# Performance work log

Hardware: AMD Instinct MI355X
Metric: run time of the kernel (lower is better)

The kernel has to match this reference:

```python
import jax, jax.numpy as jnp
import numpy as np

NHID = 256
NHEADS = 8
HEAD_F = NHID // NHEADS  # GAT per-head out_features
ALPHA = 0.1              # GAT LeakyReLU slope
NEG = -9e15


def _leaky(x, slope):
    return jnp.where(x >= 0, x, slope * x)


def _cnorm(x, axis):
    # matches Norm.compute_norm: (x - mean) / (std_unbiased + 1e-6)
    m = jnp.mean(x, axis=axis, keepdims=True)
    s = jnp.std(x, axis=axis, keepdims=True, ddof=1)
    return (x - m) / (s + 1e-6)


def _norm(x):
    # Norm('bn') forward: per-sample normalize over features (dim=1 of x[i]) then nodes (dim=0)
    return _cnorm(_cnorm(x, axis=2), axis=1)


def setup_inputs() -> dict:
    key = jax.random.key(0)
    ks = jax.random.split(key, 12)
    B, N, E, H, D = 4, 1024, NHID, NHEADS, HEAD_F

    def xavier(k, shape, gain=1.414):
        fan_in, fan_out = shape[-2], shape[-1]
        a = gain * np.sqrt(6.0 / (fan_in + fan_out))
        return jax.random.uniform(k, shape, jnp.float32, -a, a)

    return {
        "x": jax.random.normal(ks[0], (B, N, E), jnp.float32),
        "src": jax.random.normal(ks[1], (N, B, E), jnp.float32),
        "adj": jax.random.randint(ks[2], (B, N, N), 0, 2, jnp.int32),
        "Wg": xavier(ks[3], (H, E, D)),                 # per-head GAT W
        "a1": xavier(ks[4], (H, D, 1))[..., 0],         # a[:D]
        "a2": xavier(ks[5], (H, D, 1))[..., 0],         # a[D:]
        "lin_w": xavier(ks[6], (E, E), gain=1.0),
        "lin_b": jnp.zeros((E,), jnp.float32),
        "in_proj_w": xavier(ks[7], (3 * E, E), gain=1.0),
        "in_proj_b": jnp.zeros((3 * E,), jnp.float32),
        "out_proj_w": xavier(ks[8], (E, E), gain=1.0),
        "out_proj_b": jnp.zeros((E,), jnp.float32),
    }


def reference(x, src, adj, Wg, a1, a2, lin_w, lin_b, in_proj_w, in_proj_b, out_proj_w, out_proj_b):
    B, N, E = x.shape
    H, D = NHEADS, HEAD_F

    # --- multi-head dense GAT (all heads vectorized) ---
    Wh = jnp.einsum("bnf,hfd->hbnd", x, Wg)                      # [H,B,N,D]
    s1 = jnp.einsum("hbnd,hd->hbn", Wh, a1)                      # a1 . Wh_i
    s2 = jnp.einsum("hbnd,hd->hbn", Wh, a2)                      # a2 . Wh_j
    e = _leaky(s1[..., :, None] + s2[..., None, :], ALPHA)       # [H,B,N,N]
    e = jnp.where(adj[None] > 0, e, NEG)
    attn = jax.nn.softmax(e, axis=-1)                            # [H,B,N,N]
    hp = _leaky(jnp.einsum("hbnm,hbmd->hbnd", attn, Wh), 0.01)   # F.leaky_relu default

    x = x + jnp.transpose(hp, (1, 2, 0, 3)).reshape(B, N, H * D)
    e_out = jnp.mean(attn, axis=0)                               # [B,N,N]

    # --- norm1 -> linear -> norm2 ---
    x = _norm(x) @ lin_w.T + lin_b
    x = _norm(x)

    # --- nn.MultiheadAttention(query=x, key=x, value=src) ---
    srcb = jnp.transpose(src, (1, 0, 2))                         # [B,N,E]
    Wq, Wk, Wv = in_proj_w[:E], in_proj_w[E:2 * E], in_proj_w[2 * E:]
    bq, bk, bv = in_proj_b[:E], in_proj_b[E:2 * E], in_proj_b[2 * E:]
    Dh = E // H
    q = (x @ Wq.T + bq).reshape(B, N, H, Dh)
    k = (x @ Wk.T + bk).reshape(B, N, H, Dh)
    v = (srcb @ Wv.T + bv).reshape(B, N, H, Dh)
    scores = jnp.einsum("bqhd,bkhd->bhqk", q, k) / jnp.sqrt(jnp.float32(Dh))
    p = jax.nn.softmax(scores, axis=-1)
    o = jnp.einsum("bhqk,bkhd->bqhd", p, v).reshape(B, N, E)
    x = o @ out_proj_w.T + out_proj_b                            # [B,N,E]

    return (x, e_out)
```

## Files before the change

### kernel.cpp

```cpp
#include <hip/hip_runtime.h>
#include <hip/hip_bf16.h>

#define BIAS_OFF 196608
#define S1_OFF   198400
#define S2_OFF   231168
#define CS_OFF   263936
#define ST1_OFF  296704
#define ST2_OFF  298752
#define A_OFF    300800
#define MX_OFF   825088
#define RS_OFF   857856
#define PK_OFF   890624
#define B_OFF    1349376
#define C_OFF    2397952
#define FLAG_F   3446528

#define NEGC (-9.0e15f)

typedef __attribute__((ext_vector_type(8))) short bf16x8s;
typedef __attribute__((ext_vector_type(4))) float f32x4;

static __device__ __forceinline__ float bf2f(unsigned short u) {
  union { unsigned int i; float f; } v; v.i = ((unsigned int)u) << 16; return v.f;
}
static __device__ __forceinline__ unsigned short f2bf(float f) {
  union { float f; unsigned int u; } v; v.f = f;
  unsigned int r = (v.u + 0x7FFFu + ((v.u >> 16) & 1u)) >> 16;
  return (unsigned short)r;
}
static __device__ __forceinline__ float ldin(const void* p, long i, int bf) {
  return bf ? bf2f(((const unsigned short*)p)[i]) : ((const float*)p)[i];
}
static __device__ __forceinline__ unsigned short rdbf(const void* p, long i, int bf) {
  if (bf) return ((const unsigned short*)p)[i];
  return f2bf(((const float*)p)[i]);
}
static __device__ __forceinline__ void stout(void* p, long i, float v, int bf) {
  if (bf) ((unsigned short*)p)[i] = f2bf(v);
  else    ((float*)p)[i] = v;
}

__global__ __launch_bounds__(64) void detect_kernel(const unsigned short* x, int* flag) {
  int lane = threadIdx.x;
  unsigned short u = x[2 * lane];
  int e = (u >> 7) & 0xFF;
  bool good = (e >= 100 && e <= 140);
  unsigned long long m = __ballot(good);
  if (lane == 0) *flag = (__popcll(m) >= 48) ? 1 : 0;
}

__global__ __launch_bounds__(256) void packadj_kernel(const int* adj,
                                                      unsigned long long* pk) {
  int t = threadIdx.x, w = t >> 6, lane = t & 63;
  long row = blockIdx.x;
  #pragma unroll
  for (int j = 0; j < 4; ++j) {
    int m = t + 256*j;
    bool bit = adj[row*1024 + m] > 0;
    unsigned long long mask = __ballot(bit);
    if (lane == 0) pk[row*16 + w + 4*j] = mask;
  }
}

__global__ __launch_bounds__(256) void prep_kernel(
    const void* wg, const void* lin_w, const void* inp_w, const void* out_w,
    const void* lin_b, const void* inp_b, const void* out_b,
    const void* a1, const void* a2, float* ws, const int* flagp) {
  const int bf = *flagp;
  unsigned short* wbf = (unsigned short*)ws;
  int t = threadIdx.x;
  int f = blockIdx.x;
  int m = blockIdx.y;
  if (m == 0) {
    int h = t >> 5, d = t & 31;
    wbf[t*256 + f] = rdbf(wg, h*8192 + f*32 + d, bf);
  } else if (m <= 5) {
    int dst = m*65536 + t*256 + f;
    if (m == 1)      wbf[dst] = rdbf(lin_w, t*256 + f, bf);
    else if (m == 2) wbf[dst] = rdbf(inp_w, t*256 + f, bf);
    else if (m == 3) wbf[dst] = rdbf(inp_w, (256 + t)*256 + f, bf);
    else if (m == 4) wbf[dst] = rdbf(inp_w, (512 + t)*256 + f, bf);
    else             wbf[dst] = rdbf(out_w, t*256 + f, bf);
  } else {
    int h = t >> 5, d = t & 31;
    float wv = ldin(wg, h*8192 + f*32 + d, bf);
    float p1 = wv * ldin(a1, t, bf);
    float p2 = wv * ldin(a2, t, bf);
    #pragma unroll
    for (int off = 16; off > 0; off >>= 1) {
      p1 += __shfl_xor(p1, off, 32);
      p2 += __shfl_xor(p2, off, 32);
    }
    if (d == 0) {
      ws[CS_OFF + h*256 + f]        = p1;
      ws[CS_OFF + 2048 + h*256 + f] = p2;
    }
    if (f == 0) {
      ws[BIAS_OFF + t]        = ldin(lin_b, t, bf);
      ws[BIAS_OFF + 256 + t]  = ldin(inp_b, t, bf);
      ws[BIAS_OFF + 512 + t]  = ldin(inp_b, 256 + t, bf);
      ws[BIAS_OFF + 768 + t]  = ldin(inp_b, 512 + t, bf);
      ws[BIAS_OFF + 1024 + t] = ldin(out_b, t, bf);
      ws[CS_OFF + 4096 + t]   = 0.0f;
    }
  }
}

__global__ __launch_bounds__(256) void s1s2_kernel(const void* x, float* ws,
                                                   const int* flagp) {
  const int bf = *flagp;
  int t = threadIdx.x;
  int r0 = blockIdx.x * 16;
  __shared__ float X[16][260];
  __shared__ float CA[16][260];
  #pragma unroll
  for (int r = 0; r < 16; ++r)
    X[r][t] = ldin(x, (long)(r0 + r)*256 + t, bf);
  #pragma unroll
  for (int i = 0; i < 16; ++i)
    CA[i][t] = ws[CS_OFF + ((i < 8) ? i*256 : 2048 + (i - 8)*256) + t];
  __syncthreads();
  int r = t >> 4, c = t & 15;
  float acc = 0.0f;
  for (int e = 0; e < 256; ++e) acc += X[r][e] * CA[c][e];
  int row = r0 + r;
  if (c < 8) ws[S1_OFF + c*4096 + row] = acc;
  else       ws[S2_OFF + (c - 8)*4096 + row] = acc;
}

#define PB_S 1032
__global__ __launch_bounds__(512) void attn1a_kernel(const void* x, float* ws,
                                                     const int* flagp) {
  const int bf = *flagp;
  int t = threadIdx.x;
  int gid = blockIdx.x;
  int h = gid & 7;
  int b = (gid >> 3) & 3;
  int n0 = (gid >> 5) * 32;
  __shared__ __align__(16) unsigned char arena[4096 + 32*PB_S*2];
  float* s2s = (float*)arena;
  unsigned short (*Pb)[PB_S] = (unsigned short (*)[PB_S])(arena + 4096);
  float (*opart)[32][17] = (float (*)[32][17])arena;
  int w = t >> 6, lane = t & 63;
  int m = lane & 15, quad = lane >> 4;
  const unsigned long long* pk = (const unsigned long long*)(ws + PK_OFF);
  const float* s2p = ws + S2_OFF + h*4096 + b*1024;
  #pragma unroll
  for (int j = 0; j < 2; ++j) s2s[t + 512*j] = s2p[t + 512*j];
  __syncthreads();
  #pragma unroll
  for (int rr = 0; rr < 4; ++rr) {
    int r = 4*w + rr;
    int rowi = __builtin_amdgcn_readfirstlane(b*1024 + n0 + r);
    const unsigned long long* prow = pk + (long)rowi * 16;
    float s1v = ws[S1_OFF + h*4096 + rowi];
    float p[16];
    float mx = -3.4e38f;
    #pragma unroll
    for (int j = 0; j < 16; ++j) {
      int mm = lane + 64*j;
      float ev = s1v + s2s[mm];
      ev = (ev >= 0.0f) ? ev : 0.1f*ev;
      ev = ((prow[j] >> lane) & 1ull) ? ev : NEGC;
      p[j] = ev;
      mx = fmaxf(mx, ev);
    }
    #pragma unroll
    for (int off = 32; off > 0; off >>= 1) mx = fmaxf(mx, __shfl_xor(mx, off));
    float s = 0.0f;
    #pragma unroll
    for (int j = 0; j < 16; ++j) { p[j] = __expf(p[j] - mx); s += p[j]; }
    #pragma unroll
    for (int off = 32; off > 0; off >>= 1) s += __shfl_xor(s, off);
    float rs = 1.0f / s;
    #pragma unroll
    for (int j = 0; j < 16; ++j)
      Pb[r][lane + 64*j] = f2bf(p[j] * rs);
    if (lane == 0) {
      ws[MX_OFF + h*4096 + rowi] = mx;
      ws[RS_OFF + h*4096 + rowi] = rs;
    }
  }
  __syncthreads();
  f32x4 g0, g1;
  {
    const unsigned short* wht = (const unsigned short*)(ws + A_OFF);
    int ntile = w & 1;
    int ktbase = (w >> 1) * 8;
    int vd = ntile*16 + m;
    const unsigned short* wrow = wht + ((long)((b*8 + h)*32 + vd))*1024;
    f32x4 a0g0 = {0,0,0,0}, a1g0 = {0,0,0,0};
    f32x4 a0g1 = {0,0,0,0}, a1g1 = {0,0,0,0};
    #pragma unroll
    for (int kt2 = 0; kt2 < 4; ++kt2) {
      int kt = ktbase + 2*kt2;
      bf16x8s bw0 = *(const bf16x8s*)(wrow + kt*32 + quad*8);
      bf16x8s bw1 = *(const bf16x8s*)(wrow + (kt+1)*32 + quad*8);
      bf16x8s p00 = *(const bf16x8s*)&Pb[m][kt*32 + quad*8];
      bf16x8s p01 = *(const bf16x8s*)&Pb[16 + m][kt*32 + quad*8];
      a0g0 = __builtin_amdgcn_mfma_f32_16x16x32_bf16(p00, bw0, a0g0, 0, 0, 0);
      a0g1 = __builtin_amdgcn_mfma_f32_16x16x32_bf16(p01, bw0, a0g1, 0, 0, 0);
      bf16x8s p10 = *(const bf16x8s*)&Pb[m][(kt+1)*32 + quad*8];
      bf16x8s p11 = *(const bf16x8s*)&Pb[16 + m][(kt+1)*32 + quad*8];
      a1g0 = __builtin_amdgcn_mfma_f32_16x16x32_bf16(p10, bw1, a1g0, 0, 0, 0);
      a1g1 = __builtin_amdgcn_mfma_f32_16x16x32_bf16(p11, bw1, a1g1, 0, 0, 0);
    }
    g0 = a0g0 + a1g0;
    g1 = a0g1 + a1g1;
  }
  __syncthreads();
  #pragma unroll
  for (int i = 0; i < 4; ++i) {
    opart[w][quad*4 + i][m]      = g0[i];
    opart[w][16 + quad*4 + i][m] = g1[i];
  }
  __syncthreads();
  #pragma unroll
  for (int half = 0; half < 2; ++half) {
    int r = (t >> 5) + half*16;
    int dd = t & 31;
    int nt = dd >> 4, c = dd & 15;
    float sum = opart[nt][r][c] + opart[nt + 2][r][c]
              + opart[nt + 4][r][c] + opart[nt + 6][r][c];
    float hv = (sum >= 0.0f) ? sum : 0.01f*sum;
    long idx = (long)(b*1024 + n0 + r)*256 + h*32 + dd;
    ws[C_OFF + idx] = ldin(x, idx, bf) + hv;
  }
}

__global__ __launch_bounds__(256) void eout_kernel(float* ws, void* dout,
                                                   const int* flagp) {
  const int bf = *flagp;
  int t = threadIdx.x;
  int gid = blockIdx.x;
  int b = gid & 3;
  int n = gid >> 2;
  int row = b*1024 + n;
  int w = t >> 6, lane = t & 63;
  __shared__ float part[8];
  const unsigned long long* pk = (const unsigned long long*)(ws + PK_OFF);
  const unsigned long long* prow = pk + (long)row * 16;
  float v = ws[C_OFF + (long)row*256 + t];
  float s = v;
  #pragma unroll
  for (int off = 32; off > 0; off >>= 1) s += __shfl_xor(s, off);
  if (lane == 0) part[w] = s;
  __syncthreads();
  float mean = (part[0] + part[1] + part[2] + part[3]) * (1.0f/256.0f);
  float d = v - mean;
  float ss = d*d;
  #pragma unroll
  for (int off = 32; off > 0; off >>= 1) ss += __shfl_xor(ss, off);
  if (lane == 0) part[4 + w] = ss;
  __syncthreads();
  float inv = 1.0f / (sqrtf((part[4]+part[5]+part[6]+part[7]) * (1.0f/255.0f)) + 1e-6f);
  ws[B_OFF + (long)row*256 + t] = d * inv;
  float s1v[8], mxv[8], rsv[8];
  #pragma unroll
  for (int h = 0; h < 8; ++h) {
    s1v[h] = ws[S1_OFF + h*4096 + row];
    mxv[h] = ws[MX_OFF + h*4096 + row];
    rsv[h] = ws[RS_OFF + h*4096 + row];
  }
  const float* s2b = ws + S2_OFF + b*1024;
  #pragma unroll
  for (int j = 0; j < 4; ++j) {
    int m = t + 256*j;
    bool a = (prow[w + 4*j] >> lane) & 1ull;
    float acc = 0.0f;
    #pragma unroll
    for (int h = 0; h < 8; ++h) {
      float ev = s1v[h] + s2b[h*4096 + m];
      ev = (ev >= 0.0f) ? ev : 0.1f*ev;
      ev = a ? ev : NEGC;
      acc += rsv[h] * __expf(ev - mxv[h]);
    }
    stout(dout, 1048576L + (long)row*1024 + m, 0.125f*acc, bf);
  }
}

__global__ __launch_bounds__(256) void colstatsA_kernel(const float* in, float* cs) {
  int t = threadIdx.x;
  int j = blockIdx.x & 63;
  int b = blockIdx.x >> 6;
  float s = 0, ss = 0;
  for (int n = j*16; n < j*16 + 16; ++n) {
    float v = in[(b*1024 + n)*256 + t];
    s += v; ss += v*v;
  }
  cs[(b*64 + j)*256 + t] = s;
  cs[65536 + (b*64 + j)*256 + t] = ss;
}

__global__ __launch_bounds__(256) void colstatsB_kernel(const float* cs, float* st) {
  int t = threadIdx.x;
  int b = blockIdx.x;
  float s = 0, ss = 0;
  for (int j = 0; j < 64; ++j) {
    s  += cs[(b*64 + j)*256 + t];
    ss += cs[65536 + (b*64 + j)*256 + t];
  }
  float mean = s * (1.0f/1024.0f);
  float var = fmaxf((ss - s*mean) * (1.0f/1023.0f), 0.0f);
  st[b*256 + t] = mean;
  st[1024 + b*256 + t] = 1.0f / (sqrtf(var) + 1e-6f);
}

template<int IN_MODE, int RN, int OUTM, int CS>
__global__ __launch_bounds__(512) void gemm2_kernel(const void* inp,
    const unsigned short* wmat, const unsigned short* wmat2,
    const float* bias, const float* bias2, const float* st,
    void* outp, float* csout, const int* flagp) {
  const int bf = *flagp;
  int t = threadIdx.x;
  int gid = blockIdx.x;
  int rowg = (CS == 2) ? (gid >> 1) : gid;
  int colbase = (CS == 2) ? ((gid & 1) * 128) : 0;
  int r0 = rowg * 16;
  __shared__ __align__(16) unsigned short Usm[2*16*264];
  unsigned short (*Uh)[264] = (unsigned short (*)[264])Usm;
  unsigned short (*Ul)[264] = (unsigned short (*)[264])(Usm + 16*264);
  {
    int srow = t >> 5;
    int e0 = (t & 31) * 8;
    long grow = r0 + srow;
    float v[8];
    if (IN_MODE == 0) {
      #pragma unroll
      for (int j = 0; j < 8; ++j) v[j] = ldin(inp, grow*256 + e0 + j, bf);
    } else if (IN_MODE == 1) {
      int b = (int)(grow >> 10);
      const float* ip = (const float*)inp + grow*256 + e0;
      const float* mp = st + b*256 + e0;
      const float* vp = st + 1024 + b*256 + e0;
      #pragma unroll
      for (int j = 0; j < 8; ++j) v[j] = (ip[j] - mp[j]) * vp[j];
    } else if (IN_MODE == 2) {
      int b = (int)(grow >> 10), n = (int)(grow & 1023);
      #pragma unroll
      for (int j = 0; j < 8; ++j)
        v[j] = ldin(inp, (long)(n*4 + b)*256 + e0 + j, bf);
    } else {
      int b = (int)(grow >> 10), n = (int)(grow & 1023);
      const float* ip = (const float*)inp
          + ((long)(b*8 + (e0 >> 5))*1024 + n)*32 + (e0 & 31);
      #pragma unroll
      for (int j = 0; j < 8; ++j) v[j] = ip[j];
    }
    unsigned short hv[8], lv[8];
    #pragma unroll
    for (int j = 0; j < 8; ++j) {
      hv[j] = f2bf(v[j]);
      lv[j] = f2bf(v[j] - bf2f(hv[j]));
    }
    *(bf16x8s*)&Uh[srow][e0] = *(bf16x8s*)hv;
    *(bf16x8s*)&Ul[srow][e0] = *(bf16x8s*)lv;
  }
  __syncthreads();
  int w = t >> 6, lane = t & 63, m = lane & 15, quad = lane >> 4;
  const int NT = (CS == 1) ? 2 : 1;
  f32x4 accs[2];
  f32x4 acck;
  #pragma unroll
  for (int nt = 0; nt < NT; ++nt) {
    int o = colbase + w*16 + nt*128 + m;
    const unsigned short* wp = wmat + o*256 + quad*8;
    f32x4 ah_acc = {0,0,0,0}, al_acc = {0,0,0,0};
    f32x4 kh_acc = {0,0,0,0}, kl_acc = {0,0,0,0};
    const unsigned short* wp2 = (OUTM == 5) ? (wmat2 + o*256 + quad*8) : wp;
    #pragma unroll
    for (int kt = 0; kt < 8; ++kt) {
      bf16x8s ah = *(const bf16x8s*)&Uh[m][kt*32 + quad*8];
      bf16x8s al = *(const bf16x8s*)&Ul[m][kt*32 + quad*8];
      bf16x8s bw = *(const bf16x8s*)(wp + kt*32);
      ah_acc = __builtin_amdgcn_mfma_f32_16x16x32_bf16(ah, bw, ah_acc, 0, 0, 0);
      al_acc = __builtin_amdgcn_mfma_f32_16x16x32_bf16(al, bw, al_acc, 0, 0, 0);
      if (OUTM == 5) {
        bf16x8s bw2 = *(const bf16x8s*)(wp2 + kt*32);
        kh_acc = __builtin_amdgcn_mfma_f32_16x16x32_bf16(ah, bw2, kh_acc, 0, 0, 0);
        kl_acc = __builtin_amdgcn_mfma_f32_16x16x32_bf16(al, bw2, kl_acc, 0, 0, 0);
      }
    }
    accs[nt] = ah_acc + al_acc;
    if (OUTM == 5) acck = kh_acc + kl_acc;
    if (RN == 0) {
      float bv = bias[o];
      if constexpr (OUTM == 0) {
        #pragma unroll
        for (int i = 0; i < 4; ++i) {
          long row = r0 + quad*4 + i;
          ((float*)outp)[row*256 + o] = accs[nt][i] + bv;
        }
      } else if constexpr (OUTM == 1) {
        #pragma unroll
        for (int i = 0; i < 4; ++i) {
          long row = r0 + quad*4 + i;
          stout(outp, row*256 + o, accs[nt][i] + bv, bf);
        }
      } else if constexpr (OUTM == 4) {
        int h = o >> 5, d = o & 31;
        #pragma unroll
        for (int i = 0; i < 4; ++i) {
          long row = r0 + quad*4 + i;
          int b = (int)(row >> 10), n = (int)(row & 1023);
          ((unsigned short*)outp)[((long)((b*8 + h)*32 + d))*1024 + n]
              = f2bf(accs[nt][i] + bv);
        }
      } else if constexpr (OUTM == 5) {
        float* wsf = (float*)outp;
        float* qhm = wsf + A_OFF;
        unsigned short* khm = (unsigned short*)(wsf + B_OFF);
        float bq = bias[o], bk = bias2[o];
        int h = o >> 5, d = o & 31;
        #pragma unroll
        for (int i = 0; i < 4; ++i) {
          long row = r0 + quad*4 + i;
          int b = (int)(row >> 10), n = (int)(row & 1023);
          long idx = ((long)((b*8 + h)*1024 + n))*32 + d;
          qhm[idx] = accs[nt][i] + bq;
          khm[idx] = f2bf(acck[i] + bk);
        }
      }
    }
  }
  if constexpr (RN == 1) {
    __syncthreads();
    float (*O)[264] = (float (*)[264])Usm;
    #pragma unroll
    for (int nt = 0; nt < NT; ++nt) {
      int oc = colbase + w*16 + nt*128 + m;
      float bv = bias[oc];
      #pragma unroll
      for (int i = 0; i < 4; ++i)
        O[quad*4 + i][oc] = accs[nt][i] + bv;
    }
    __syncthreads();
    #pragma unroll
    for (int rr = 0; rr < 2; ++rr) {
      int r = 2*w + rr;
      float vals[4]; float s = 0.0f;
      #pragma unroll
      for (int j = 0; j < 4; ++j) { vals[j] = O[r][lane + 64*j]; s += vals[j]; }
      #pragma unroll
      for (int off = 32; off > 0; off >>= 1) s += __shfl_xor(s, off);
      float mean = s * (1.0f/256.0f);
      float ss = 0.0f;
      #pragma unroll
      for (int j = 0; j < 4; ++j) { float d = vals[j] - mean; ss += d*d; }
      #pragma unroll
      for (int off = 32; off > 0; off >>= 1) ss += __shfl_xor(ss, off);
      float inv = 1.0f / (sqrtf(ss * (1.0f/255.0f)) + 1e-6f);
      #pragma unroll
      for (int j = 0; j < 4; ++j) {
        float nv = (vals[j] - mean) * inv;
        ((float*)outp)[(long)(r0 + r)*256 + lane + 64*j] = nv;
        O[r][lane + 64*j] = nv;
      }
    }
    __syncthreads();
    if (csout != nullptr && t < 256) {
      float s = 0, ss = 0;
      #pragma unroll
      for (int r = 0; r < 16; ++r) { float v = O[r][t]; s += v; ss += v*v; }
      csout[gid*256 + t] = s;
      csout[65536 + gid*256 + t] = ss;
    }
  }
}

#define SPS 1036
__global__ __launch_bounds__(512) void attn2_kernel(float* ws) {
  int t = threadIdx.x;
  int gid = blockIdx.x;
  int h = gid & 7;
  int b = (gid >> 3) & 3;
  int n0 = (gid >> 5) << 4;
  __shared__ __align__(16) float Sp[16*SPS];
  __shared__ __align__(16) float opart[8][16][17];
  float* qq = ws + A_OFF;
  const unsigned short* kk = (const unsigned short*)(ws + B_OFF);
  const unsigned short* vt = (const unsigned short*)(ws + C_OFF);
  int base_bh = (b*8 + h)*1024;
  int w = t >> 6, lane = t & 63;
  int m = lane & 15, quad = lane >> 4;
  const float scl = 0.17677669529663687f;
  {
    const float* qp = qq + (base_bh + n0 + m)*32 + quad*8;
    bf16x8s aq;
    #pragma unroll
    for (int j = 0; j < 8; ++j) ((unsigned short*)&aq)[j] = f2bf(qp[j]);
    f32x4 zero = {0.0f, 0.0f, 0.0f, 0.0f};
    #pragma unroll
    for (int kt = 0; kt < 8; ++kt) {
      int kbase = w*128 + kt*16;
      bf16x8s bk = *(const bf16x8s*)(kk + (base_bh + kbase + m)*32 + quad*8);
      f32x4 d = __builtin_amdgcn_mfma_f32_16x16x32_bf16(aq, bk, zero, 0, 0, 0);
      int key = kbase + m;
      #pragma unroll
      for (int i = 0; i < 4; ++i)
        Sp[(quad*4 + i)*SPS + key] = d[i] * scl;
    }
  }
  __syncthreads();
  #pragma unroll
  for (int rr = 0; rr < 2; ++rr) {
    int r = 2*w + rr;
    float* Sr = Sp + r*SPS;
    float p[16];
    #pragma unroll
    for (int j = 0; j < 16; ++j) p[j] = Sr[lane + 64*j];
    float mx = -3.4e38f;
    #pragma unroll
    for (int j = 0; j < 16; ++j) mx = fmaxf(mx, p[j]);
    #pragma unroll
    for (int off = 32; off > 0; off >>= 1) mx = fmaxf(mx, __shfl_xor(mx, off));
    float s = 0.0f;
    #pragma unroll
    for (int j = 0; j < 16; ++j) { p[j] = __expf(p[j] - mx); s += p[j]; }
    #pragma unroll
    for (int off = 32; off > 0; off >>= 1) s += __shfl_xor(s, off);
    float rs = 1.0f / s;
    unsigned short* Pr = (unsigned short*)Sr;
    #pragma unroll
    for (int j = 0; j < 16; ++j)
      Pr[lane + 64*j] = f2bf(p[j] * rs);
  }
  __syncthreads();
  {
    int ntile = w & 1;
    int ktbase = (w >> 1) * 8;
    int vd = ntile*16 + m;
    const unsigned short* vrow = vt + base_bh*32 + vd*1024;
    const unsigned short* P0 = (const unsigned short*)Sp + m*(SPS*2);
    f32x4 acc0 = {0.0f, 0.0f, 0.0f, 0.0f};
    f32x4 acc1 = {0.0f, 0.0f, 0.0f, 0.0f};
    #pragma unroll
    for (int kt2 = 0; kt2 < 4; ++kt2) {
      int kt = ktbase + 2*kt2;
      bf16x8s ap0 = *(const bf16x8s*)(P0 + kt*32 + quad*8);
      bf16x8s bv0 = *(const bf16x8s*)(vrow + kt*32 + quad*8);
      acc0 = __builtin_amdgcn_mfma_f32_16x16x32_bf16(ap0, bv0, acc0, 0, 0, 0);
      bf16x8s ap1 = *(const bf16x8s*)(P0 + (kt+1)*32 + quad*8);
      bf16x8s bv1 = *(const bf16x8s*)(vrow + (kt+1)*32 + quad*8);
      acc1 = __builtin_amdgcn_mfma_f32_16x16x32_bf16(ap1, bv1, acc1, 0, 0, 0);
    }
    f32x4 acc = acc0 + acc1;
    #pragma unroll
    for (int i = 0; i < 4; ++i)
      opart[w][quad*4 + i][m] = acc[i];
  }
  __syncthreads();
  {
    int r = t >> 5, d = t & 31;
    int nt = d >> 4, c = d & 15;
    float sum = opart[nt][r][c] + opart[nt + 2][r][c]
              + opart[nt + 4][r][c] + opart[nt + 6][r][c];
    qq[(base_bh + n0 + r)*32 + d] = sum;
  }
}

extern "C" void kernel_launch(void* const* d_in, const int* in_sizes, int n_in,
                              void* d_out, int out_size, void* d_ws, size_t ws_size,
                              hipStream_t stream) {
  const void* x   = d_in[0];
  const void* src = d_in[1];
  const int* adj  = (const int*)d_in[2];
  const void* wg  = d_in[3];
  const void* a1  = d_in[4];
  const void* a2  = d_in[5];
  const void* lw  = d_in[6];
  const void* lb  = d_in[7];
  const void* ipw = d_in[8];
  const void* ipb = d_in[9];
  const void* opw = d_in[10];
  const void* opb = d_in[11];
  float* ws = (float*)d_ws;
  const unsigned short* wbf = (const unsigned short*)d_ws;
  int* flagp = (int*)(ws + FLAG_F);

  detect_kernel<<<1, 64, 0, stream>>>((const unsigned short*)x, flagp);
  prep_kernel<<<dim3(256, 7), 256, 0, stream>>>(wg, lw, ipw, opw, lb, ipb, opb,
                                                a1, a2, ws, flagp);
  packadj_kernel<<<4096, 256, 0, stream>>>(adj,
      (unsigned long long*)(ws + PK_OFF));
  gemm2_kernel<0,0,4,2><<<512, 512, 0, stream>>>(x, wbf + 0*65536,
      nullptr, ws + CS_OFF + 4096, nullptr, nullptr, ws + A_OFF, nullptr,
      flagp);
  s1s2_kernel<<<256, 256, 0, stream>>>(x, ws, flagp);
  attn1a_kernel<<<1024, 512, 0, stream>>>(x, ws, flagp);
  eout_kernel<<<4096, 256, 0, stream>>>(ws, d_out, flagp);
  colstatsA_kernel<<<256, 256, 0, stream>>>(ws + B_OFF, ws + MX_OFF);
  colstatsB_kernel<<<4, 256, 0, stream>>>(ws + MX_OFF, ws + ST1_OFF);
  gemm2_kernel<1,1,0,1><<<256, 512, 0, stream>>>(ws + B_OFF, wbf + 1*65536,
      nullptr, ws + BIAS_OFF, nullptr, ws + ST1_OFF, ws + C_OFF, ws + MX_OFF,
      flagp);
  colstatsB_kernel<<<4, 256, 0, stream>>>(ws + MX_OFF, ws + ST2_OFF);
  gemm2_kernel<1,0,5,2><<<512, 512, 0, stream>>>(ws + C_OFF, wbf + 2*65536,
      wbf + 3*65536, ws + BIAS_OFF + 256, ws + BIAS_OFF + 512, ws + ST2_OFF,
      ws, nullptr, flagp);
  gemm2_kernel<2,0,4,2><<<512, 512, 0, stream>>>(src, wbf + 4*65536,
      nullptr, ws + BIAS_OFF + 768, nullptr, nullptr, ws + C_OFF, nullptr,
      flagp);
  attn2_kernel<<<2048, 512, 0, stream>>>(ws);
  gemm2_kernel<3,0,1,2><<<512, 512, 0, stream>>>(ws + A_OFF, wbf + 5*65536,
      nullptr, ws + BIAS_OFF + 1024, nullptr, nullptr, d_out, nullptr,
      flagp);
}
```

Baseline: 245.6 us.

## Fuse GAT score projections into Wh GEMM epilogue and keep attn2 scores in registers

New measurement: 243.2 us. Within noise of the previous version (-1.0%).

```diff
diff --git a/kernel.cpp b/kernel.cpp
--- a/kernel.cpp
+++ b/kernel.cpp
@@ -81,51 +81,16 @@
     else if (m == 3) wbf[dst] = rdbf(inp_w, (256 + t)*256 + f, bf);
     else if (m == 4) wbf[dst] = rdbf(inp_w, (512 + t)*256 + f, bf);
     else             wbf[dst] = rdbf(out_w, t*256 + f, bf);
-  } else {
-    int h = t >> 5, d = t & 31;
-    float wv = ldin(wg, h*8192 + f*32 + d, bf);
-    float p1 = wv * ldin(a1, t, bf);
-    float p2 = wv * ldin(a2, t, bf);
-    #pragma unroll
-    for (int off = 16; off > 0; off >>= 1) {
-      p1 += __shfl_xor(p1, off, 32);
-      p2 += __shfl_xor(p2, off, 32);
-    }
-    if (d == 0) {
-      ws[CS_OFF + h*256 + f]        = p1;
-      ws[CS_OFF + 2048 + h*256 + f] = p2;
-    }
-    if (f == 0) {
-      ws[BIAS_OFF + t]        = ldin(lin_b, t, bf);
-      ws[BIAS_OFF + 256 + t]  = ldin(inp_b, t, bf);
-      ws[BIAS_OFF + 512 + t]  = ldin(inp_b, 256 + t, bf);
-      ws[BIAS_OFF + 768 + t]  = ldin(inp_b, 512 + t, bf);
-      ws[BIAS_OFF + 1024 + t] = ldin(out_b, t, bf);
-      ws[CS_OFF + 4096 + t]   = 0.0f;
-    }
-  }
-}
-
-__global__ __launch_bounds__(256) void s1s2_kernel(const void* x, float* ws,
-                                                   const int* flagp) {
-  const int bf = *flagp;
-  int t = threadIdx.x;
-  int r0 = blockIdx.x * 16;
-  __shared__ float X[16][260];
-  __shared__ float CA[16][260];
-  #pragma unroll
-  for (int r = 0; r < 16; ++r)
-    X[r][t] = ldin(x, (long)(r0 + r)*256 + t, bf);
-  #pragma unroll
-  for (int i = 0; i < 16; ++i)
-    CA[i][t] = ws[CS_OFF + ((i < 8) ? i*256 : 2048 + (i - 8)*256) + t];
-  __syncthreads();
-  int r = t >> 4, c = t & 15;
-  float acc = 0.0f;
-  for (int e = 0; e < 256; ++e) acc += X[r][e] * CA[c][e];
-  int row = r0 + r;
-  if (c < 8) ws[S1_OFF + c*4096 + row] = acc;
-  else       ws[S2_OFF + (c - 8)*4096 + row] = acc;
+  } else if (f == 0) {
+    ws[BIAS_OFF + t]        = ldin(lin_b, t, bf);
+    ws[BIAS_OFF + 256 + t]  = ldin(inp_b, t, bf);
+    ws[BIAS_OFF + 512 + t]  = ldin(inp_b, 256 + t, bf);
+    ws[BIAS_OFF + 768 + t]  = ldin(inp_b, 512 + t, bf);
+    ws[BIAS_OFF + 1024 + t] = ldin(out_b, t, bf);
+    ws[BIAS_OFF + 1280 + t] = ldin(a1, t, bf);
+    ws[BIAS_OFF + 1536 + t] = ldin(a2, t, bf);
+    ws[CS_OFF + 4096 + t]   = 0.0f;
+  }
 }
 
 #define PB_S 1032
@@ -306,7 +271,7 @@
   st[1024 + b*256 + t] = 1.0f / (sqrtf(var) + 1e-6f);
 }
 
-template<int IN_MODE, int RN, int OUTM, int CS>
+template<int IN_MODE, int RN, int OUTM, int CS, int SOP>
 __global__ __launch_bounds__(512) void gemm2_kernel(const void* inp,
     const unsigned short* wmat, const unsigned short* wmat2,
     const float* bias, const float* bias2, const float* st,
@@ -423,6 +388,34 @@
       }
     }
   }
+  if constexpr (SOP == 1) {
+    __shared__ float sp[2][8][16];
+    int o = colbase + w*16 + m;
+    float a1v = bias2[o];
+    float a2v = st[o];
+    #pragma unroll
+    for (int i = 0; i < 4; ++i) {
+      float v1 = accs[0][i] * a1v;
+      float v2 = accs[0][i] * a2v;
+      #pragma unroll
+      for (int off = 8; off > 0; off >>= 1) {
+        v1 += __shfl_xor(v1, off);
+        v2 += __shfl_xor(v2, off);
+      }
+      if (m == 0) {
+        sp[0][w][quad*4 + i] = v1;
+        sp[1][w][quad*4 + i] = v2;
+      }
+    }
+    __syncthreads();
+    if (t < 128) {
+      int which = t >> 6, h2 = (t >> 4) & 3, r = t & 15;
+      float v = sp[which][2*h2][r] + sp[which][2*h2 + 1][r];
+      long dst = (which ? S2_OFF : S1_OFF)
+               + (long)((colbase >> 5) + h2)*4096 + (r0 + r);
+      csout[dst] = v;
+    }
+  }
   if constexpr (RN == 1) {
     __syncthreads();
     float (*O)[264] = (float (*)[264])Usm;
@@ -468,14 +461,18 @@
   }
 }
 
-#define SPS 1036
+#define P2S 1036
 __global__ __launch_bounds__(512) void attn2_kernel(float* ws) {
   int t = threadIdx.x;
   int gid = blockIdx.x;
   int h = gid & 7;
   int b = (gid >> 3) & 3;
   int n0 = (gid >> 5) << 4;
-  __shared__ __align__(16) float Sp[16*SPS];
+  __shared__ __align__(16) unsigned short P[16][P2S];
+  __shared__ float pmx[8][16];
+  __shared__ float psm[8][16];
+  __shared__ float gmx[16];
+  __shared__ float grs[16];
   __shared__ __align__(16) float opart[8][16][17];
   float* qq = ws + A_OFF;
   const unsigned short* kk = (const unsigned short*)(ws + B_OFF);
@@ -484,6 +481,7 @@
   int w = t >> 6, lane = t & 63;
   int m = lane & 15, quad = lane >> 4;
   const float scl = 0.17677669529663687f;
+  float s[8][4];
   {
     const float* qp = qq + (base_bh + n0 + m)*32 + quad*8;
     bf16x8s aq;
@@ -495,35 +493,43 @@
       int kbase = w*128 + kt*16;
       bf16x8s bk = *(const bf16x8s*)(kk + (base_bh + kbase + m)*32 + quad*8);
       f32x4 d = __builtin_amdgcn_mfma_f32_16x16x32_bf16(aq, bk, zero, 0, 0, 0);
-      int key = kbase + m;
-      #pragma unroll
-      for (int i = 0; i < 4; ++i)
-        Sp[(quad*4 + i)*SPS + key] = d[i] * scl;
-    }
-  }
-  __syncthreads();
-  #pragma unroll
-  for (int rr = 0; rr < 2; ++rr) {
-    int r = 2*w + rr;
-    float* Sr = Sp + r*SPS;
-    float p[16];
-    #pragma unroll
-    for (int j = 0; j < 16; ++j) p[j] = Sr[lane + 64*j];
-    float mx = -3.4e38f;
-    #pragma unroll
-    for (int j = 0; j < 16; ++j) mx = fmaxf(mx, p[j]);
-    #pragma unroll
-    for (int off = 32; off > 0; off >>= 1) mx = fmaxf(mx, __shfl_xor(mx, off));
-    float s = 0.0f;
-    #pragma unroll
-    for (int j = 0; j < 16; ++j) { p[j] = __expf(p[j] - mx); s += p[j]; }
-    #pragma unroll
-    for (int off = 32; off > 0; off >>= 1) s += __shfl_xor(s, off);
-    float rs = 1.0f / s;
-    unsigned short* Pr = (unsigned short*)Sr;
-    #pragma unroll
-    for (int j = 0; j < 16; ++j)
-      Pr[lane + 64*j] = f2bf(p[j] * rs);
+      #pragma unroll
+      for (int i = 0; i < 4; ++i) s[kt][i] = d[i] * scl;
+    }
+  }
+  #pragma unroll
+  for (int i = 0; i < 4; ++i) {
+    float mx = s[0][i];
+    #pragma unroll
+    for (int kt = 1; kt < 8; ++kt) mx = fmaxf(mx, s[kt][i]);
+    #pragma unroll
+    for (int off = 8; off > 0; off >>= 1) mx = fmaxf(mx, __shfl_xor(mx, off));
+    float sm = 0.0f;
+    #pragma unroll
+    for (int kt = 0; kt < 8; ++kt) sm += __expf(s[kt][i] - mx);
+    #pragma unroll
+    for (int off = 8; off > 0; off >>= 1) sm += __shfl_xor(sm, off);
+    if (m == 0) { pmx[w][quad*4 + i] = mx; psm[w][quad*4 + i] = sm; }
+  }
+  __syncthreads();
+  if (t < 16) {
+    float mx = pmx[0][t];
+    #pragma unroll
+    for (int w2 = 1; w2 < 8; ++w2) mx = fmaxf(mx, pmx[w2][t]);
+    float den = 0.0f;
+    #pragma unroll
+    for (int w2 = 0; w2 < 8; ++w2) den += psm[w2][t] * __expf(pmx[w2][t] - mx);
+    gmx[t] = mx;
+    grs[t] = 1.0f / den;
+  }
+  __syncthreads();
+  #pragma unroll
+  for (int i = 0; i < 4; ++i) {
+    int row = quad*4 + i;
+    float mx = gmx[row], rs = grs[row];
+    #pragma unroll
+    for (int kt = 0; kt < 8; ++kt)
+      P[row][w*128 + kt*16 + m] = f2bf(__expf(s[kt][i] - mx) * rs);
   }
   __syncthreads();
   {
@@ -531,7 +537,7 @@
     int ktbase = (w >> 1) * 8;
     int vd = ntile*16 + m;
     const unsigned short* vrow = vt + base_bh*32 + vd*1024;
-    const unsigned short* P0 = (const unsigned short*)Sp + m*(SPS*2);
+    const unsigned short* P0 = &P[m][0];
     f32x4 acc0 = {0.0f, 0.0f, 0.0f, 0.0f};
     f32x4 acc1 = {0.0f, 0.0f, 0.0f, 0.0f};
     #pragma unroll
@@ -583,26 +589,25 @@
                                                 a1, a2, ws, flagp);
   packadj_kernel<<<4096, 256, 0, stream>>>(adj,
       (unsigned long long*)(ws + PK_OFF));
-  gemm2_kernel<0,0,4,2><<<512, 512, 0, stream>>>(x, wbf + 0*65536,
-      nullptr, ws + CS_OFF + 4096, nullptr, nullptr, ws + A_OFF, nullptr,
-      flagp);
-  s1s2_kernel<<<256, 256, 0, stream>>>(x, ws, flagp);
+  gemm2_kernel<0,0,4,2,1><<<512, 512, 0, stream>>>(x, wbf + 0*65536,
+      nullptr, ws + CS_OFF + 4096, ws + BIAS_OFF + 1280, ws + BIAS_OFF + 1536,
+      ws + A_OFF, ws, flagp);
   attn1a_kernel<<<1024, 512, 0, stream>>>(x, ws, flagp);
   eout_kernel<<<4096, 256, 0, stream>>>(ws, d_out, flagp);
   colstatsA_kernel<<<256, 256, 0, stream>>>(ws + B_OFF, ws + MX_OFF);
   colstatsB_kernel<<<4, 256, 0, stream>>>(ws + MX_OFF, ws + ST1_OFF);
-  gemm2_kernel<1,1,0,1><<<256, 512, 0, stream>>>(ws + B_OFF, wbf + 1*65536,
+  gemm2_kernel<1,1,0,1,0><<<256, 512, 0, stream>>>(ws + B_OFF, wbf + 1*65536,
       nullptr, ws + BIAS_OFF, nullptr, ws + ST1_OFF, ws + C_OFF, ws + MX_OFF,
       flagp);
   colstatsB_kernel<<<4, 256, 0, stream>>>(ws + MX_OFF, ws + ST2_OFF);
-  gemm2_kernel<1,0,5,2><<<512, 512, 0, stream>>>(ws + C_OFF, wbf + 2*65536,
+  gemm2_kernel<1,0,5,2,0><<<512, 512, 0, stream>>>(ws + C_OFF, wbf + 2*65536,
       wbf + 3*65536, ws + BIAS_OFF + 256, ws + BIAS_OFF + 512, ws + ST2_OFF,
       ws, nullptr, flagp);
-  gemm2_kernel<2,0,4,2><<<512, 512, 0, stream>>>(src, wbf + 4*65536,
+  gemm2_kernel<2,0,4,2,0><<<512, 512, 0, stream>>>(src, wbf + 4*65536,
       nullptr, ws + BIAS_OFF + 768, nullptr, nullptr, ws + C_OFF, nullptr,
       flagp);
   attn2_kernel<<<2048, 512, 0, stream>>>(ws);
-  gemm2_kernel<3,0,1,2><<<512, 512, 0, stream>>>(ws + A_OFF, wbf + 5*65536,
+  gemm2_kernel<3,0,1,2,0><<<512, 512, 0, stream>>>(ws + A_OFF, wbf + 5*65536,
       nullptr, ws + BIAS_OFF + 1024, nullptr, nullptr, d_out, nullptr,
       flagp);
 }
```
